# Performance work log

Measured on AMD Instinct MI355X. Metric: run time of the kernel, lower is better.

## Reference

```python
import jax, jax.numpy as jnp
import numpy as np

B, H, W = 32, 768, 768
POS_THR = 0.1
NEG_RATIO = 3
TOPK_NO_POS = 500


def setup_inputs() -> dict:
    key = jax.random.key(0)
    k1, k2, k3 = jax.random.split(key, 3)
    pred = jax.random.uniform(k1, (B, H, W, 2), dtype=jnp.float32)
    region_scores = jax.random.uniform(k2, (B, H, W), dtype=jnp.float32) ** 16
    affinity_scores = jax.random.uniform(k3, (B, H, W), dtype=jnp.float32) ** 16
    return {"pred": pred, "region_scores": region_scores, "affinity_scores": affinity_scores}


def _single_image_loss(pre_loss, label):
    # Vectorized OHEM: replaces the per-sample Python loop + torch.topk.
    b = pre_loss.shape[0]
    loss = pre_loss.reshape(b, -1)   # [B, N]
    lab = label.reshape(b, -1)       # [B, N]
    n = loss.shape[1]
    pos = lab >= POS_THR             # [B, N] bool
    p = jnp.sum(pos, axis=1)         # positive pixel count per sample
    pos_sum = jnp.sum(jnp.where(pos, loss, 0.0), axis=1)
    posi_loss = jnp.where(p > 0, pos_sum / jnp.maximum(p, 1).astype(loss.dtype), 0.0)
    # Negatives sorted descending; -inf pushes positives to the tail.
    # When p == 0 the mask is all-False so this sorts the full loss vector,
    # matching torch.topk(pre_loss[i], 500).
    neg_vals = jnp.where(pos, -jnp.inf, loss)
    sorted_desc = jnp.flip(jnp.sort(neg_vals, axis=1), axis=1)
    nn = n - p                       # negative count
    # mean of all negatives when nn < 3p == mean of top-min(nn,3p); else top-3p
    k = jnp.where(p > 0, jnp.minimum(nn, NEG_RATIO * p), TOPK_NO_POS)
    csum = jnp.cumsum(jnp.where(jnp.isfinite(sorted_desc), sorted_desc, 0.0), axis=1)
    topk_sum = jnp.take_along_axis(csum, jnp.maximum(k - 1, 0)[:, None], axis=1)[:, 0]
    nega_loss = jnp.where(k > 0, topk_sum / jnp.maximum(k, 1).astype(loss.dtype), 0.0)
    return jnp.sum(posi_loss + nega_loss)


def reference(pred, region_scores, affinity_scores):
    p_gh = pred[..., 0]
    p_gah = pred[..., 1]
    loss1 = (p_gh - region_scores) ** 2   # MSELoss(reduction='none')
    loss2 = (p_gah - affinity_scores) ** 2
    char_loss = _single_image_loss(loss1, region_scores)
    affi_loss = _single_image_loss(loss2, affinity_scores)
    b = pred.shape[0]
    return char_loss / b + affi_loss / b
```

## Files before the change

### kernel.cpp

```cpp
#include <hip/hip_runtime.h>


constexpr int   BATCH   = 32;
constexpr int   NPS     = 768 * 768;
constexpr int   CH2     = BATCH * 2;
constexpr int   EPB     = 8192;
constexpr int   BX      = NPS / EPB;
constexpr float POS_THR_F = 0.1f;
constexpr unsigned TOPK_NO_POS = 500u;
constexpr int   NB1     = 2048;
constexpr int   CAP     = 131072;
constexpr int   CAPB    = 1024;

__global__ __launch_bounds__(256, 8) void k_hist(
    const float4* __restrict__ pred4,
    const float4* __restrict__ reg4,
    const float4* __restrict__ aff4,
    unsigned* __restrict__ h1c,
    unsigned* __restrict__ pcnt, float* __restrict__ psum)
{
    __shared__ unsigned sc0[NB1], sc1[NB1];
    __shared__ unsigned wpc[8];
    __shared__ float    wps[8];
    for (int j = threadIdx.x; j < NB1; j += 256) { sc0[j] = 0u; sc1[j] = 0u; }
    __syncthreads();

    const int  b   = blockIdx.y;
    const int  tid = threadIdx.x;
    constexpr int ITERS = EPB / 1024;
    long idx4 = (((long)b * NPS + (long)blockIdx.x * EPB) >> 2) + tid;

    unsigned pc0 = 0, pc1 = 0;
    float    ps0 = 0.f, ps1 = 0.f;

    for (int i = 0; i < ITERS; ++i) {
        const float4 r  = reg4[idx4];
        const float4 a  = aff4[idx4];
        const float4 pA = pred4[idx4 * 2];
        const float4 pB = pred4[idx4 * 2 + 1];
#define DO_PIX(RR, AA, PG, PA) do {                                           \
        float d0 = (PG) - (RR); float v0 = d0 * d0;                           \
        if ((RR) >= POS_THR_F) { pc0++; ps0 += v0; }                          \
        else atomicAdd(&sc0[__float_as_uint(v0) >> 19], 1u);                  \
        float d1 = (PA) - (AA); float v1 = d1 * d1;                           \
        if ((AA) >= POS_THR_F) { pc1++; ps1 += v1; }                          \
        else atomicAdd(&sc1[__float_as_uint(v1) >> 19], 1u);                  \
    } while (0)
        DO_PIX(r.x, a.x, pA.x, pA.y);
        DO_PIX(r.y, a.y, pA.z, pA.w);
        DO_PIX(r.z, a.z, pB.x, pB.y);
        DO_PIX(r.w, a.w, pB.z, pB.w);
#undef DO_PIX
        idx4 += 256;
    }
    __syncthreads();

    for (int j = tid; j < NB1; j += 256) {
        unsigned c0 = sc0[j];
        if (c0) atomicAdd(&h1c[(b*2+0)*NB1 + j], c0);
        unsigned c1 = sc1[j];
        if (c1) atomicAdd(&h1c[(b*2+1)*NB1 + j], c1);
    }
    for (int o = 32; o > 0; o >>= 1) {
        pc0 += __shfl_down(pc0, o); ps0 += __shfl_down(ps0, o);
        pc1 += __shfl_down(pc1, o); ps1 += __shfl_down(ps1, o);
    }
    const int wid = tid >> 6, lane = tid & 63;
    if (lane == 0) { wpc[wid] = pc0; wps[wid] = ps0; wpc[4+wid] = pc1; wps[4+wid] = ps1; }
    __syncthreads();
    if (tid == 0) {
        unsigned t0 = 0, t1 = 0; float s0 = 0.f, s1 = 0.f;
        for (int q = 0; q < 4; ++q) { t0 += wpc[q]; s0 += wps[q]; t1 += wpc[4+q]; s1 += wps[4+q]; }
        atomicAdd(&pcnt[b*2+0], t0); unsafeAtomicAdd(&psum[b*2+0], s0);
        atomicAdd(&pcnt[b*2+1], t1); unsafeAtomicAdd(&psum[b*2+1], s1);
    }
}

template<int NBINS>
__device__ __forceinline__ void select_counts(
    const unsigned* cnt, unsigned k, unsigned& outBin, unsigned& outRem)
{
    constexpr int PER = NBINS / 256;
    const int t = threadIdx.x;
    unsigned lc[PER];
#pragma unroll
    for (int j = 0; j < PER; ++j) lc[j] = cnt[t*PER + j];
    unsigned lsum = 0;
#pragma unroll
    for (int j = 0; j < PER; ++j) lsum += lc[j];

    __shared__ unsigned part[256];
    __shared__ unsigned s_bin, s_rem;
    part[t] = lsum;
    __syncthreads();
    for (int off = 1; off < 256; off <<= 1) {
        unsigned v = (t + off < 256) ? part[t + off] : 0u;
        __syncthreads();
        part[t] += v;
        __syncthreads();
    }
    unsigned cum = (t + 1 < 256) ? part[t + 1] : 0u;
#pragma unroll
    for (int j = PER - 1; j >= 0; --j) {
        unsigned c = lc[j];
        if (cum < k && k <= cum + c) { s_bin = (unsigned)(t * PER + j); s_rem = k - cum; }
        cum += c;
    }
    __syncthreads();
    outBin = s_bin; outRem = s_rem;
}

__global__ __launch_bounds__(256) void k_scan1(
    const unsigned* __restrict__ h1c,
    const unsigned* __restrict__ pcnt, const float* __restrict__ psum,
    unsigned* __restrict__ T1, unsigned* __restrict__ rem1,
    unsigned* __restrict__ kk, float* __restrict__ posi)
{
    const int idx = blockIdx.x;
    const unsigned p  = pcnt[idx];
    const unsigned nn = (unsigned)NPS - p;
    const unsigned k  = p ? ((nn < 3u*p) ? nn : 3u*p) : TOPK_NO_POS;
    if (threadIdx.x == 0) {
        kk[idx]   = k;
        posi[idx] = p ? (psum[idx] / (float)p) : 0.0f;
    }
    if (k == 0u) {
        if (threadIdx.x == 0) { T1[idx] = 0xFFFFFFFFu; rem1[idx] = 0u; }
        return;
    }
    unsigned bin, rem;
    select_counts<NB1>(h1c + idx*NB1, k, bin, rem);
    if (threadIdx.x == 0) { T1[idx] = bin; rem1[idx] = rem; }
}

__global__ __launch_bounds__(256, 8) void k_compact(
    const float4* __restrict__ pred4,
    const float4* __restrict__ reg4,
    const float4* __restrict__ aff4,
    const unsigned* __restrict__ T1,
    float* __restrict__ cbuf, unsigned* __restrict__ ccnt,
    double* __restrict__ sumAbove)
{
    __shared__ float    lb0[CAPB], lb1[CAPB];
    __shared__ unsigned lcnt[2];
    __shared__ unsigned sbase[2];
    __shared__ float    wred[8];
    if (threadIdx.x < 2) lcnt[threadIdx.x] = 0u;
    __syncthreads();

    const int b = blockIdx.y;
    const unsigned t1r = T1[b*2+0], t1a = T1[b*2+1];
    const int tid = threadIdx.x, lane = tid & 63;
    float*    gb0 = cbuf + (size_t)(b*2+0) * CAP;
    float*    gb1 = cbuf + (size_t)(b*2+1) * CAP;
    unsigned* gc0 = ccnt + b*2+0;
    unsigned* gc1 = ccnt + b*2+1;
    float rs0 = 0.f, rs1 = 0.f;

    auto proc = [&](float tgt, float pg, unsigned t1, float& rs,
                    unsigned* lcnt_p, float* lbuf, unsigned* gcnt, float* gbuf) {
        if (tgt >= POS_THR_F) return;
        const float d = pg - tgt;
        const float v = d * d;
        const unsigned key = __float_as_uint(v) >> 19;
        if (key > t1) { rs += v; return; }
        if (key != t1) return;
        const unsigned long long m = __ballot(true);
        const int ldr = __ffsll(m) - 1;
        const unsigned pre = (unsigned)__popcll(m & ((1ull << lane) - 1ull));
        unsigned base = 0;
        if (lane == ldr) base = atomicAdd(lcnt_p, (unsigned)__popcll(m));
        base = __shfl(base, ldr);
        const unsigned ix = base + pre;
        if (ix < (unsigned)CAPB) lbuf[ix] = v;
        else { unsigned g = atomicAdd(gcnt, 1u); if (g < (unsigned)CAP) gbuf[g] = v; }
    };

    constexpr int ITERS = EPB / 1024;
    long idx4 = (((long)b * NPS + (long)blockIdx.x * EPB) >> 2) + tid;

    for (int i = 0; i < ITERS; ++i) {
        const float4 r  = reg4[idx4];
        const float4 a  = aff4[idx4];
        const float4 pA = pred4[idx4 * 2];
        const float4 pB = pred4[idx4 * 2 + 1];
        proc(r.x, pA.x, t1r, rs0, &lcnt[0], lb0, gc0, gb0);
        proc(r.y, pA.z, t1r, rs0, &lcnt[0], lb0, gc0, gb0);
        proc(r.z, pB.x, t1r, rs0, &lcnt[0], lb0, gc0, gb0);
        proc(r.w, pB.z, t1r, rs0, &lcnt[0], lb0, gc0, gb0);
        proc(a.x, pA.y, t1a, rs1, &lcnt[1], lb1, gc1, gb1);
        proc(a.y, pA.w, t1a, rs1, &lcnt[1], lb1, gc1, gb1);
        proc(a.z, pB.y, t1a, rs1, &lcnt[1], lb1, gc1, gb1);
        proc(a.w, pB.w, t1a, rs1, &lcnt[1], lb1, gc1, gb1);
        idx4 += 256;
    }
    __syncthreads();

    const unsigned lc0 = lcnt[0] < (unsigned)CAPB ? lcnt[0] : (unsigned)CAPB;
    const unsigned lc1 = lcnt[1] < (unsigned)CAPB ? lcnt[1] : (unsigned)CAPB;
    if (tid == 0)      sbase[0] = lc0 ? atomicAdd(gc0, lc0) : 0u;
    else if (tid == 1) sbase[1] = lc1 ? atomicAdd(gc1, lc1) : 0u;
    __syncthreads();
    for (unsigned i = tid; i < lc0; i += 256) {
        unsigned g = sbase[0] + i;
        if (g < (unsigned)CAP) gb0[g] = lb0[i];
    }
    for (unsigned i = tid; i < lc1; i += 256) {
        unsigned g = sbase[1] + i;
        if (g < (unsigned)CAP) gb1[g] = lb1[i];
    }
    for (int o = 32; o > 0; o >>= 1) { rs0 += __shfl_down(rs0, o); rs1 += __shfl_down(rs1, o); }
    const int wid = tid >> 6;
    if (lane == 0) { wred[wid] = rs0; wred[4+wid] = rs1; }
    __syncthreads();
    if (tid == 0) {
        float s0 = wred[0]+wred[1]+wred[2]+wred[3];
        float s1 = wred[4]+wred[5]+wred[6]+wred[7];
        unsafeAtomicAdd(&sumAbove[b*2+0], (double)s0);
        unsafeAtomicAdd(&sumAbove[b*2+1], (double)s1);
    }
}

__global__ __launch_bounds__(256) void k_refine(
    const float* __restrict__ cbuf, const unsigned* __restrict__ ccnt,
    const unsigned* __restrict__ T1, const unsigned* __restrict__ rem1,
    const unsigned* __restrict__ kk, const float* __restrict__ posi,
    const double* __restrict__ sumAbove,
    float* __restrict__ contrib)
{
    const int ch = blockIdx.x;
    const unsigned k = kk[ch];
    if (k == 0u) {
        if (threadIdx.x == 0) contrib[ch] = posi[ch];
        return;
    }
    unsigned cnt = ccnt[ch];
    if (cnt > (unsigned)CAP) cnt = (unsigned)CAP;
    const float* buf = cbuf + (size_t)ch * CAP;
    const int tid = threadIdx.x;

    __shared__ unsigned hA[NB1];
    __shared__ unsigned hB[256];
    __shared__ double   wsum[4];
    for (int j = tid; j < NB1; j += 256) hA[j] = 0u;
    __syncthreads();
    for (unsigned i = tid; i < cnt; i += 256) {
        const unsigned bt = __float_as_uint(buf[i]);
        atomicAdd(&hA[(bt >> 8) & 2047u], 1u);
    }
    __syncthreads();
    unsigned T2, rem2;
    select_counts<NB1>(hA, rem1[ch], T2, rem2);

    hB[tid] = 0u;
    __syncthreads();
    for (unsigned i = tid; i < cnt; i += 256) {
        const unsigned bt = __float_as_uint(buf[i]);
        if (((bt >> 8) & 2047u) == T2) atomicAdd(&hB[bt & 255u], 1u);
    }
    __syncthreads();
    unsigned T3, rem3;
    select_counts<256>(hB, rem2, T3, rem3);

    const float t = __uint_as_float((T1[ch] << 19) | (T2 << 8) | T3);
    double s = 0.0;
    for (unsigned i = tid; i < cnt; i += 256) {
        const float v = buf[i];
        if (v > t) s += (double)v;
    }
    for (int o = 32; o > 0; o >>= 1) s += __shfl_down(s, o);
    const int wid = tid >> 6, lane = tid & 63;
    if (lane == 0) wsum[wid] = s;
    __syncthreads();
    if (tid == 0) {
        const double stop = wsum[0] + wsum[1] + wsum[2] + wsum[3];
        const double nega = (sumAbove[ch] + stop + (double)rem3 * (double)t) / (double)k;
        contrib[ch] = (float)((double)posi[ch] + nega);
    }
}

__global__ void k_reduce(const float* __restrict__ contrib, float* __restrict__ out)
{
    double v = (double)contrib[threadIdx.x];
    for (int o = 32; o > 0; o >>= 1) v += __shfl_down(v, o);
    if (threadIdx.x == 0) out[0] = (float)(v / (double)BATCH);
}

extern "C" void kernel_launch(void* const* d_in, const int* in_sizes, int n_in,
                              void* d_out, int out_size, void* d_ws, size_t ws_size,
                              hipStream_t stream)
{
    (void)in_sizes; (void)n_in; (void)out_size; (void)ws_size;
    const float4* pred4 = (const float4*)d_in[0];
    const float4* reg4  = (const float4*)d_in[1];
    const float4* aff4  = (const float4*)d_in[2];

    char* w = (char*)d_ws;
    unsigned* h1c  = (unsigned*)w;
    unsigned* pcnt = h1c + (size_t)CH2 * NB1;
    float*    psum = (float*)(pcnt + CH2);
    unsigned* T1   = (unsigned*)(psum + CH2);
    unsigned* rem1 = T1 + CH2;
    unsigned* kk   = rem1 + CH2;
    float*    posi = (float*)(kk + CH2);
    float*    contrib = posi + CH2;
    unsigned* ccnt = (unsigned*)(contrib + CH2);
    double*   sumAbove = (double*)(ccnt + CH2);
    const size_t hdr_bytes = (size_t)((char*)(sumAbove + CH2) - w);

    float* cbuf = (float*)(w + ((size_t)1 << 20));

    hipMemsetAsync(d_ws, 0, hdr_bytes, stream);

    dim3 grid(BX, BATCH);
    k_hist<<<grid, 256, 0, stream>>>(pred4, reg4, aff4, h1c, pcnt, psum);
    k_scan1<<<CH2, 256, 0, stream>>>(h1c, pcnt, psum, T1, rem1, kk, posi);
    k_compact<<<grid, 256, 0, stream>>>(pred4, reg4, aff4, T1, cbuf, ccnt, sumAbove);
    k_refine<<<CH2, 256, 0, stream>>>(cbuf, ccnt, T1, rem1, kk, posi, sumAbove, contrib);
    k_reduce<<<1, 64, 0, stream>>>(contrib, (float*)d_out);
}
```

Measured before the change: 415.0 us.

## Use per-thread packed byte histograms with coarse bins and three-level radix refine

The first-pass histogram shrinks to 64 coarse bins, each covering a quarter-octave with low values clamped to bin 0. Each thread counts into its own byte-packed LDS slots, so the heavily contended shared atomics go away. The per-thread counts are then reduced with wave shuffles before the global atomics. The scan becomes a single-thread loop, compaction switches from wave-aggregated to plain per-lane LDS atomics, and refine uses an 11/11/10 bit radix selection. In exchange, far more elements land in the selected coarse bin, which raises compaction and refine work and the risk of overflowing the buffer capacity, and the larger LDS footprint lowers occupancy.

```diff
diff --git a/kernel.cpp b/kernel.cpp
--- a/kernel.cpp
+++ b/kernel.cpp
@@ -8,21 +8,27 @@
 constexpr int   BX      = NPS / EPB;
 constexpr float POS_THR_F = 0.1f;
 constexpr unsigned TOPK_NO_POS = 500u;
-constexpr int   NB1     = 2048;
+constexpr int   NB1     = 64;
+constexpr int   RAW_OFF = 448;
 constexpr int   CAP     = 131072;
 constexpr int   CAPB    = 1024;
 
-__global__ __launch_bounds__(256, 8) void k_hist(
+__device__ __forceinline__ unsigned bin_of(float v) {
+    int b = (int)(__float_as_uint(v) >> 21) - RAW_OFF;
+    return b < 0 ? 0u : (unsigned)b;
+}
+
+__global__ __launch_bounds__(256, 4) void k_hist(
     const float4* __restrict__ pred4,
     const float4* __restrict__ reg4,
     const float4* __restrict__ aff4,
     unsigned* __restrict__ h1c,
     unsigned* __restrict__ pcnt, float* __restrict__ psum)
 {
-    __shared__ unsigned sc0[NB1], sc1[NB1];
+    __shared__ unsigned hist[2][16][256];
     __shared__ unsigned wpc[8];
     __shared__ float    wps[8];
-    for (int j = threadIdx.x; j < NB1; j += 256) { sc0[j] = 0u; sc1[j] = 0u; }
+    for (int j = threadIdx.x; j < 2*16*256; j += 256) ((unsigned*)hist)[j] = 0u;
     __syncthreads();
 
     const int  b   = blockIdx.y;
@@ -41,10 +47,12 @@
 #define DO_PIX(RR, AA, PG, PA) do {                                           \
         float d0 = (PG) - (RR); float v0 = d0 * d0;                           \
         if ((RR) >= POS_THR_F) { pc0++; ps0 += v0; }                          \
-        else atomicAdd(&sc0[__float_as_uint(v0) >> 19], 1u);                  \
+        else { unsigned bn = bin_of(v0);                                      \
+               atomicAdd(&hist[0][bn>>2][tid], 1u << ((bn&3)*8)); }           \
         float d1 = (PA) - (AA); float v1 = d1 * d1;                           \
         if ((AA) >= POS_THR_F) { pc1++; ps1 += v1; }                          \
-        else atomicAdd(&sc1[__float_as_uint(v1) >> 19], 1u);                  \
+        else { unsigned bn = bin_of(v1);                                      \
+               atomicAdd(&hist[1][bn>>2][tid], 1u << ((bn&3)*8)); }           \
     } while (0)
         DO_PIX(r.x, a.x, pA.x, pA.y);
         DO_PIX(r.y, a.y, pA.z, pA.w);
@@ -55,17 +63,33 @@
     }
     __syncthreads();
 
-    for (int j = tid; j < NB1; j += 256) {
-        unsigned c0 = sc0[j];
-        if (c0) atomicAdd(&h1c[(b*2+0)*NB1 + j], c0);
-        unsigned c1 = sc1[j];
-        if (c1) atomicAdd(&h1c[(b*2+1)*NB1 + j], c1);
-    }
+    const int wid = tid >> 6, lane = tid & 63;
+    for (int q = 0; q < 8; ++q) {
+        const int p  = wid * 8 + q;
+        const int ch = p >> 4, w = p & 15;
+        unsigned s = hist[ch][w][lane] + hist[ch][w][lane+64]
+                   + hist[ch][w][lane+128] + hist[ch][w][lane+192];
+        unsigned lo = s & 0x00FF00FFu;
+        unsigned hi = (s >> 8) & 0x00FF00FFu;
+        for (int o = 32; o > 0; o >>= 1) {
+            lo += __shfl_down(lo, o);
+            hi += __shfl_down(hi, o);
+        }
+        if (lane == 0) {
+            const unsigned base = (unsigned)(b*2 + ch) * NB1 + (unsigned)w * 4u;
+            unsigned c0 = lo & 0xFFFFu, c2 = lo >> 16;
+            unsigned c1 = hi & 0xFFFFu, c3 = hi >> 16;
+            if (c0) atomicAdd(&h1c[base+0], c0);
+            if (c1) atomicAdd(&h1c[base+1], c1);
+            if (c2) atomicAdd(&h1c[base+2], c2);
+            if (c3) atomicAdd(&h1c[base+3], c3);
+        }
+    }
+
     for (int o = 32; o > 0; o >>= 1) {
         pc0 += __shfl_down(pc0, o); ps0 += __shfl_down(ps0, o);
         pc1 += __shfl_down(pc1, o); ps1 += __shfl_down(ps1, o);
     }
-    const int wid = tid >> 6, lane = tid & 63;
     if (lane == 0) { wpc[wid] = pc0; wps[wid] = ps0; wpc[4+wid] = pc1; wps[4+wid] = ps1; }
     __syncthreads();
     if (tid == 0) {
@@ -110,27 +134,27 @@
     outBin = s_bin; outRem = s_rem;
 }
 
-__global__ __launch_bounds__(256) void k_scan1(
+__global__ void k_scan1(
     const unsigned* __restrict__ h1c,
     const unsigned* __restrict__ pcnt, const float* __restrict__ psum,
     unsigned* __restrict__ T1, unsigned* __restrict__ rem1,
     unsigned* __restrict__ kk, float* __restrict__ posi)
 {
+    if (threadIdx.x != 0) return;
     const int idx = blockIdx.x;
     const unsigned p  = pcnt[idx];
     const unsigned nn = (unsigned)NPS - p;
     const unsigned k  = p ? ((nn < 3u*p) ? nn : 3u*p) : TOPK_NO_POS;
-    if (threadIdx.x == 0) {
-        kk[idx]   = k;
-        posi[idx] = p ? (psum[idx] / (float)p) : 0.0f;
-    }
-    if (k == 0u) {
-        if (threadIdx.x == 0) { T1[idx] = 0xFFFFFFFFu; rem1[idx] = 0u; }
-        return;
-    }
-    unsigned bin, rem;
-    select_counts<NB1>(h1c + idx*NB1, k, bin, rem);
-    if (threadIdx.x == 0) { T1[idx] = bin; rem1[idx] = rem; }
+    kk[idx]   = k;
+    posi[idx] = p ? (psum[idx] / (float)p) : 0.0f;
+    if (k == 0u) { T1[idx] = 0xFFFFFFFFu; rem1[idx] = 0u; return; }
+    unsigned cum = 0, bin = 0, rem = k;
+    for (int j = NB1 - 1; j >= 0; --j) {
+        const unsigned c = h1c[idx*NB1 + j];
+        if (cum < k && k <= cum + c) { bin = (unsigned)j; rem = k - cum; }
+        cum += c;
+    }
+    T1[idx] = bin; rem1[idx] = rem;
 }
 
 __global__ __launch_bounds__(256, 8) void k_compact(
@@ -162,16 +186,10 @@
         if (tgt >= POS_THR_F) return;
         const float d = pg - tgt;
         const float v = d * d;
-        const unsigned key = __float_as_uint(v) >> 19;
+        const unsigned key = bin_of(v);
         if (key > t1) { rs += v; return; }
         if (key != t1) return;
-        const unsigned long long m = __ballot(true);
-        const int ldr = __ffsll(m) - 1;
-        const unsigned pre = (unsigned)__popcll(m & ((1ull << lane) - 1ull));
-        unsigned base = 0;
-        if (lane == ldr) base = atomicAdd(lcnt_p, (unsigned)__popcll(m));
-        base = __shfl(base, ldr);
-        const unsigned ix = base + pre;
+        const unsigned ix = atomicAdd(lcnt_p, 1u);
         if (ix < (unsigned)CAPB) lbuf[ix] = v;
         else { unsigned g = atomicAdd(gcnt, 1u); if (g < (unsigned)CAP) gbuf[g] = v; }
     };
@@ -223,7 +241,7 @@
 
 __global__ __launch_bounds__(256) void k_refine(
     const float* __restrict__ cbuf, const unsigned* __restrict__ ccnt,
-    const unsigned* __restrict__ T1, const unsigned* __restrict__ rem1,
+    const unsigned* __restrict__ rem1,
     const unsigned* __restrict__ kk, const float* __restrict__ posi,
     const double* __restrict__ sumAbove,
     float* __restrict__ contrib)
@@ -239,30 +257,41 @@
     const float* buf = cbuf + (size_t)ch * CAP;
     const int tid = threadIdx.x;
 
-    __shared__ unsigned hA[NB1];
-    __shared__ unsigned hB[256];
+    __shared__ unsigned h[2048];
     __shared__ double   wsum[4];
-    for (int j = tid; j < NB1; j += 256) hA[j] = 0u;
+
+    for (int j = tid; j < 1024; j += 256) h[j] = 0u;
+    __syncthreads();
+    for (unsigned i = tid; i < cnt; i += 256)
+        atomicAdd(&h[__float_as_uint(buf[i]) >> 21], 1u);
+    __syncthreads();
+    unsigned TA, remA;
+    select_counts<1024>(h, rem1[ch], TA, remA);
+    __syncthreads();
+
+    for (int j = tid; j < 2048; j += 256) h[j] = 0u;
     __syncthreads();
     for (unsigned i = tid; i < cnt; i += 256) {
         const unsigned bt = __float_as_uint(buf[i]);
-        atomicAdd(&hA[(bt >> 8) & 2047u], 1u);
-    }
-    __syncthreads();
-    unsigned T2, rem2;
-    select_counts<NB1>(hA, rem1[ch], T2, rem2);
-
-    hB[tid] = 0u;
-    __syncthreads();
+        if ((bt >> 21) == TA) atomicAdd(&h[(bt >> 10) & 2047u], 1u);
+    }
+    __syncthreads();
+    unsigned TB, remB;
+    select_counts<2048>(h, remA, TB, remB);
+    __syncthreads();
+
+    for (int j = tid; j < 1024; j += 256) h[j] = 0u;
+    __syncthreads();
+    const unsigned abPrefix = (TA << 11) | TB;
     for (unsigned i = tid; i < cnt; i += 256) {
         const unsigned bt = __float_as_uint(buf[i]);
-        if (((bt >> 8) & 2047u) == T2) atomicAdd(&hB[bt & 255u], 1u);
-    }
-    __syncthreads();
-    unsigned T3, rem3;
-    select_counts<256>(hB, rem2, T3, rem3);
-
-    const float t = __uint_as_float((T1[ch] << 19) | (T2 << 8) | T3);
+        if ((bt >> 10) == abPrefix) atomicAdd(&h[bt & 1023u], 1u);
+    }
+    __syncthreads();
+    unsigned TC, rem3;
+    select_counts<1024>(h, remB, TC, rem3);
+
+    const float t = __uint_as_float((TA << 21) | (TB << 10) | TC);
     double s = 0.0;
     for (unsigned i = tid; i < cnt; i += 256) {
         const float v = buf[i];
@@ -314,8 +343,8 @@
 
     dim3 grid(BX, BATCH);
     k_hist<<<grid, 256, 0, stream>>>(pred4, reg4, aff4, h1c, pcnt, psum);
-    k_scan1<<<CH2, 256, 0, stream>>>(h1c, pcnt, psum, T1, rem1, kk, posi);
+    k_scan1<<<CH2, 64, 0, stream>>>(h1c, pcnt, psum, T1, rem1, kk, posi);
     k_compact<<<grid, 256, 0, stream>>>(pred4, reg4, aff4, T1, cbuf, ccnt, sumAbove);
-    k_refine<<<CH2, 256, 0, stream>>>(cbuf, ccnt, T1, rem1, kk, posi, sumAbove, contrib);
+    k_refine<<<CH2, 256, 0, stream>>>(cbuf, ccnt, rem1, kk, posi, sumAbove, contrib);
     k_reduce<<<1, 64, 0, stream>>>(contrib, (float*)d_out);
 }
```

New measurement: 499.3 us. +20.3%, slower.
